# Kernel optimization log

Measured on AMD Instinct MI355X. Metric: run time of the kernel, lower is better.

Reference implementation:

```python
import jax, jax.numpy as jnp
import numpy as np


def _shift(x, n):
    # torch.roll along the last (angular) axis
    return jnp.roll(x, n, axis=3)


def _flip(x, n):
    # mirror about index n along the last axis: out[..., i] = x[..., (n - i) mod W]
    return jnp.roll(jnp.flip(x, axis=3), n + 1, axis=3)


def setup_inputs() -> dict:
    key = jax.random.key(0)
    k1, k2, k3 = jax.random.split(key, 3)
    B, C, H, W = 16, 96, 96, 96
    x = jax.random.normal(k1, (B, C, H, W), dtype=jnp.float32)
    s = jax.random.normal(k2, (B, 5), dtype=jnp.float32)
    w = jax.random.uniform(k3, (B, C, H, W), dtype=jnp.float32) + 0.1  # keep denominator well-conditioned
    return {"x": x, "s": s, "w": w}


def reference(x, s, w):
    # s.shape[1] == 5 branch of SymmetryControl (square symmetry: 3 rotations + 2 mirrors)
    sg = jax.nn.sigmoid(s).reshape(s.shape[0], -1, 1, 1)  # [B,5,1,1]
    step = x.shape[3] // 8

    x90 = _shift(x, step * 2)
    x180 = _shift(x, step * 4)
    x270 = _shift(x, step * 6)
    x90f = _flip(x, step * 2 - 1)
    x180f = _flip(x, step * 4 - 1)

    w90 = sg[:, 0:1] * _shift(w, step * 2)
    w180 = sg[:, 1:2] * _shift(w, step * 4)
    w270 = sg[:, 2:3] * _shift(w, step * 6)
    w90f = sg[:, 3:4] * _flip(w, step * 2 - 1)
    w180f = sg[:, 4:5] * _flip(w, step * 4 - 1)

    a = (w * x + w90 * x90 + w180 * x180 + w270 * x270
         + w90f * x90f + w180f * x180f)
    b = w + w90 + w180 + w270 + w90f + w180f
    return a / b
```

## Files before the change

kernel.cpp:

```cpp
#include <hip/hip_runtime.h>


#define WDIM 96
#define ROWS_PER_BLOCK 8

__global__ __launch_bounds__(WDIM * ROWS_PER_BLOCK)
void symctl_kernel(const float* __restrict__ x,
                   const float* __restrict__ s,
                   const float* __restrict__ w,
                   float* __restrict__ out,
                   int n_rows, int rows_per_batch) {
    const int i   = threadIdx.x;
    const int row = blockIdx.x * ROWS_PER_BLOCK + threadIdx.y;
    if (row >= n_rows) return;

    const int b = row / rows_per_batch;
    const float* sb = s + b * 5;
    const float sg0 = 1.0f / (1.0f + __expf(-sb[0]));
    const float sg1 = 1.0f / (1.0f + __expf(-sb[1]));
    const float sg2 = 1.0f / (1.0f + __expf(-sb[2]));
    const float sg3 = 1.0f / (1.0f + __expf(-sb[3]));
    const float sg4 = 1.0f / (1.0f + __expf(-sb[4]));

    int i24 = i - 24; if (i24 < 0) i24 += WDIM;
    int i48 = i - 48; if (i48 < 0) i48 += WDIM;
    int i72 = i - 72; if (i72 < 0) i72 += WDIM;
    int f23 = 23 - i; if (f23 < 0) f23 += WDIM;
    int f47 = 47 - i; if (f47 < 0) f47 += WDIM;

    const long base = (long)row * WDIM;
    const float* __restrict__ xr = x + base;
    const float* __restrict__ wr = w + base;

    const float x0 = xr[i],   w0 = wr[i];
    const float xa = xr[i24], wa = wr[i24];
    const float xb = xr[i48], wb = wr[i48];
    const float xc = xr[i72], wc = wr[i72];
    const float xd = xr[f23], wd = wr[f23];
    const float xe = xr[f47], we = wr[f47];

    const float num = w0 * x0
                    + sg0 * (wa * xa)
                    + sg1 * (wb * xb)
                    + sg2 * (wc * xc)
                    + sg3 * (wd * xd)
                    + sg4 * (we * xe);
    const float den = w0
                    + sg0 * wa
                    + sg1 * wb
                    + sg2 * wc
                    + sg3 * wd
                    + sg4 * we;

    out[base + i] = num / den;
}

extern "C" void kernel_launch(void* const* d_in, const int* in_sizes, int n_in,
                              void* d_out, int out_size, void* d_ws, size_t ws_size,
                              hipStream_t stream) {
    const float* x = (const float*)d_in[0];
    const float* s = (const float*)d_in[1];
    const float* w = (const float*)d_in[2];
    float* out = (float*)d_out;

    const int n_rows = in_sizes[0] / WDIM;
    const int rows_per_batch = 96 * 96;
    const int grid = (n_rows + ROWS_PER_BLOCK - 1) / ROWS_PER_BLOCK;

    dim3 block(WDIM, ROWS_PER_BLOCK);
    symctl_kernel<<<grid, block, 0, stream>>>(x, s, w, out, n_rows, rows_per_batch);
}
```

Measured before the change: 183.6 us.

## Vectorize row loads to float4 with quad-level rotation and mirror indexing

Each thread now handles four consecutive elements via float4 loads. The rotations (multiples of 24) and mirrors (about 23 and 47) map to whole-quad offsets, with mirrored quads read in reverse lane order. Sigmoids are computed once per block into shared memory, and the division becomes a fast reciprocal multiply. Block shape changes to 24x32 and the bounds check is dropped. This assumes the row count divides by 32 and trades an exact divide for an approximate reciprocal.

```diff
diff --git a/kernel.cpp b/kernel.cpp
--- a/kernel.cpp
+++ b/kernel.cpp
@@ -2,57 +2,67 @@
 
 
 #define WDIM 96
-#define ROWS_PER_BLOCK 8
+#define QDIM 24
+#define ROWS 32
+#define RPB  9216
 
-__global__ __launch_bounds__(WDIM * ROWS_PER_BLOCK)
+__global__ __launch_bounds__(QDIM * ROWS)
 void symctl_kernel(const float* __restrict__ x,
                    const float* __restrict__ s,
                    const float* __restrict__ w,
-                   float* __restrict__ out,
-                   int n_rows, int rows_per_batch) {
-    const int i   = threadIdx.x;
-    const int row = blockIdx.x * ROWS_PER_BLOCK + threadIdx.y;
-    if (row >= n_rows) return;
+                   float* __restrict__ out) {
+    const int qx  = threadIdx.x;
+    const int row = blockIdx.x * ROWS + threadIdx.y;
+    const int b   = (blockIdx.x * ROWS) / RPB;
 
-    const int b = row / rows_per_batch;
-    const float* sb = s + b * 5;
-    const float sg0 = 1.0f / (1.0f + __expf(-sb[0]));
-    const float sg1 = 1.0f / (1.0f + __expf(-sb[1]));
-    const float sg2 = 1.0f / (1.0f + __expf(-sb[2]));
-    const float sg3 = 1.0f / (1.0f + __expf(-sb[3]));
-    const float sg4 = 1.0f / (1.0f + __expf(-sb[4]));
+    __shared__ float sg[5];
+    const int flat = threadIdx.y * QDIM + qx;
+    if (flat < 5) sg[flat] = 1.0f / (1.0f + __expf(-s[b * 5 + flat]));
+    __syncthreads();
+    const float sg0 = sg[0], sg1 = sg[1], sg2 = sg[2], sg3 = sg[3], sg4 = sg[4];
 
-    int i24 = i - 24; if (i24 < 0) i24 += WDIM;
-    int i48 = i - 48; if (i48 < 0) i48 += WDIM;
-    int i72 = i - 72; if (i72 < 0) i72 += WDIM;
-    int f23 = 23 - i; if (f23 < 0) f23 += WDIM;
-    int f47 = 47 - i; if (f47 < 0) f47 += WDIM;
+    int qa = qx - 6;  if (qa < 0) qa += QDIM;
+    int qb = qx - 12; if (qb < 0) qb += QDIM;
+    int qc = qx + 6;  if (qc >= QDIM) qc -= QDIM;
+    int qd = 5  - qx; if (qd < 0) qd += QDIM;
+    int qe = 11 - qx; if (qe < 0) qe += QDIM;
 
-    const long base = (long)row * WDIM;
-    const float* __restrict__ xr = x + base;
-    const float* __restrict__ wr = w + base;
+    const float4* __restrict__ xr = (const float4*)(x + (size_t)row * WDIM);
+    const float4* __restrict__ wr = (const float4*)(w + (size_t)row * WDIM);
 
-    const float x0 = xr[i],   w0 = wr[i];
-    const float xa = xr[i24], wa = wr[i24];
-    const float xb = xr[i48], wb = wr[i48];
-    const float xc = xr[i72], wc = wr[i72];
-    const float xd = xr[f23], wd = wr[f23];
-    const float xe = xr[f47], we = wr[f47];
+    const float4 X0 = xr[qx], Xa = xr[qa], Xb = xr[qb], Xc = xr[qc], Xd = xr[qd], Xe = xr[qe];
+    const float4 W0 = wr[qx], Wa = wr[qa], Wb = wr[qb], Wc = wr[qc], Wd = wr[qd], We = wr[qe];
 
-    const float num = w0 * x0
-                    + sg0 * (wa * xa)
-                    + sg1 * (wb * xb)
-                    + sg2 * (wc * xc)
-                    + sg3 * (wd * xd)
-                    + sg4 * (we * xe);
-    const float den = w0
-                    + sg0 * wa
-                    + sg1 * wb
-                    + sg2 * wc
-                    + sg3 * wd
-                    + sg4 * we;
+    const float* x0p = (const float*)&X0; const float* w0p = (const float*)&W0;
+    const float* xap = (const float*)&Xa; const float* wap = (const float*)&Wa;
+    const float* xbp = (const float*)&Xb; const float* wbp = (const float*)&Wb;
+    const float* xcp = (const float*)&Xc; const float* wcp = (const float*)&Wc;
+    const float* xdp = (const float*)&Xd; const float* wdp = (const float*)&Wd;
+    const float* xep = (const float*)&Xe; const float* wep = (const float*)&We;
 
-    out[base + i] = num / den;
+    float4 res;
+    float* rp = (float*)&res;
+#pragma unroll
+    for (int j = 0; j < 4; ++j) {
+        const int r = 3 - j;
+        const float w0 = w0p[j], wa = wap[j], wb = wbp[j], wc = wcp[j];
+        const float wd = wdp[r], we = wep[r];
+        const float ga = sg0 * wa, gb = sg1 * wb, gc = sg2 * wc;
+        const float gd = sg3 * wd, ge = sg4 * we;
+
+        float num = w0 * x0p[j];
+        num = fmaf(ga, xap[j], num);
+        num = fmaf(gb, xbp[j], num);
+        num = fmaf(gc, xcp[j], num);
+        num = fmaf(gd, xdp[r], num);
+        num = fmaf(ge, xep[r], num);
+
+        const float den = w0 + ga + gb + gc + gd + ge;
+        rp[j] = num * __builtin_amdgcn_rcpf(den);
+    }
+
+    float4* outr = (float4*)(out + (size_t)row * WDIM);
+    outr[qx] = res;
 }
 
 extern "C" void kernel_launch(void* const* d_in, const int* in_sizes, int n_in,
@@ -64,9 +74,8 @@
     float* out = (float*)d_out;
 
     const int n_rows = in_sizes[0] / WDIM;
-    const int rows_per_batch = 96 * 96;
-    const int grid = (n_rows + ROWS_PER_BLOCK - 1) / ROWS_PER_BLOCK;
+    const int grid = n_rows / ROWS;
 
-    dim3 block(WDIM, ROWS_PER_BLOCK);
-    symctl_kernel<<<grid, block, 0, stream>>>(x, s, w, out, n_rows, rows_per_batch);
+    dim3 block(QDIM, ROWS);
+    symctl_kernel<<<grid, block, 0, stream>>>(x, s, w, out);
 }
```

Result: faster. 157.9 us (-14.0%).
